# Performance work log

Measured on AMD Instinct MI355X. Metric: run time of the kernel, lower is better.

Reference implementation:

```python
import jax, jax.numpy as jnp
import numpy as np

C = 512
NH = 4
HD = C // NH
G = 32  # min(32, C) and C % 32 == 0
EPS = 1e-5


def setup_inputs() -> dict:
    key = jax.random.key(0)
    ks = jax.random.split(key, 11)
    s = 1.0 / np.sqrt(C)
    return {
        "x": jax.random.normal(ks[0], (16, C, 32, 32), dtype=jnp.float32),
        "gamma": jnp.ones((C,), jnp.float32),
        "beta": jnp.zeros((C,), jnp.float32),
        "wq": jax.random.normal(ks[1], (C, C), jnp.float32) * s,
        "bq": jax.random.normal(ks[2], (C,), jnp.float32) * 0.01,
        "wk": jax.random.normal(ks[3], (C, C), jnp.float32) * s,
        "bk": jax.random.normal(ks[4], (C,), jnp.float32) * 0.01,
        "wv": jax.random.normal(ks[5], (C, C), jnp.float32) * s,
        "bv": jax.random.normal(ks[6], (C,), jnp.float32) * 0.01,
        "wp": jax.random.normal(ks[7], (C, C), jnp.float32) * s,
        "bp": jax.random.normal(ks[8], (C,), jnp.float32) * 0.01,
    }


def _group_norm(x, gamma, beta):
    b, c, h, w = x.shape
    xr = x.reshape(b, G, c // G, h, w)
    mean = xr.mean(axis=(2, 3, 4), keepdims=True)
    var = xr.var(axis=(2, 3, 4), keepdims=True)
    xn = ((xr - mean) * jax.lax.rsqrt(var + EPS)).reshape(b, c, h, w)
    return xn * gamma[None, :, None, None] + beta[None, :, None, None]


def _conv1x1(x, w, b):
    # 1x1 conv == per-position channel GEMM
    return jnp.einsum('oc,bchw->bohw', w, x) + b[None, :, None, None]


def reference(x, gamma, beta, wq, bq, wk, bk, wv, bv, wp, bp):
    b, c, h, w = x.shape
    hw = h * w
    scale = HD ** (-0.5)
    hn = _group_norm(x, gamma, beta)
    q = _conv1x1(hn, wq, bq).reshape(b, NH, HD, hw)
    k = _conv1x1(hn, wk, bk).reshape(b, NH, HD, hw)
    v = _conv1x1(hn, wv, bv).reshape(b, NH, HD, hw)
    attn = jnp.einsum('bhdq,bhdk->bhqk', q, k) * scale  # [b, nh, hw, hw]
    attn = jax.nn.softmax(attn, axis=-1)
    out = jnp.einsum('bhqk,bhdk->bhdq', attn, v)  # [b, nh, hd, hw]
    out = out.reshape(b, c, h, w)
    out = _conv1x1(out, wp, bp)
    return x + out
```

## Files before the change

### kernel.cpp

```cpp
#include <hip/hip_runtime.h>
#include <math.h>

#define CCH 512
#define NH 4
#define HD 128
#define HW 1024
#define BATCH 16
#define EPS 1e-5f

typedef __attribute__((ext_vector_type(8))) short bfrag;
typedef __attribute__((ext_vector_type(4))) float f4;

static __device__ __forceinline__ unsigned short f2bf(float f) {
  union { float f; unsigned u; } v;
  v.f = f;
  unsigned r = v.u + 0x7fff + ((v.u >> 16) & 1);
  return (unsigned short)(r >> 16);
}
static __device__ __forceinline__ unsigned pack2(unsigned short a, unsigned short b) {
  return (unsigned)a | ((unsigned)b << 16);
}
static __device__ __forceinline__ void ldg_lds16(const unsigned short* g,
                                                 unsigned short* l) {
  __builtin_amdgcn_global_load_lds(
      (const __attribute__((address_space(1))) unsigned int*)g,
      (__attribute__((address_space(3))) unsigned int*)l, 16, 0, 0);
}

__global__ __launch_bounds__(256) void wcvt_kernel(const float* __restrict__ s0,
                                                   const float* __restrict__ s1,
                                                   const float* __restrict__ s2,
                                                   const float* __restrict__ s3,
                                                   unsigned short* __restrict__ d) {
  const float* srcs[4] = {s0, s1, s2, s3};
  const float* s = srcs[blockIdx.y];
  unsigned short* dp = d + (size_t)blockIdx.y * CCH * CCH;
  int i = blockIdx.x * 256 + threadIdx.x;
  f4 v = ((const f4*)s)[i];
  ushort4 o;
  o.x = f2bf(v.x); o.y = f2bf(v.y); o.z = f2bf(v.z); o.w = f2bf(v.w);
  ((ushort4*)dp)[i] = o;
}

__global__ __launch_bounds__(256) void gn_kernel(const float* __restrict__ x,
                                                 const float* __restrict__ gamma,
                                                 const float* __restrict__ beta,
                                                 unsigned short* __restrict__ hn) {
  int b = blockIdx.x >> 5, g = blockIdx.x & 31;
  const float* xp = x + ((size_t)b * CCH + g * 16) * HW;
  int t = threadIdx.x;
  float s = 0.f, ss = 0.f;
  const f4* xp4 = (const f4*)xp;
  for (int i = t; i < 4096; i += 256) {
    f4 v = xp4[i];
    s += v.x + v.y + v.z + v.w;
    ss += v.x * v.x + v.y * v.y + v.z * v.z + v.w * v.w;
  }
#pragma unroll
  for (int off = 32; off > 0; off >>= 1) {
    s += __shfl_xor(s, off);
    ss += __shfl_xor(ss, off);
  }
  __shared__ float rs[4], rss[4];
  int w = t >> 6;
  if ((t & 63) == 0) { rs[w] = s; rss[w] = ss; }
  __syncthreads();
  s = rs[0] + rs[1] + rs[2] + rs[3];
  ss = rss[0] + rss[1] + rss[2] + rss[3];
  const float invn = 1.f / (16 * HW);
  float mean = s * invn;
  float var = ss * invn - mean * mean;
  float rstd = rsqrtf(var + EPS);
  float a_[16], b_[16];
#pragma unroll
  for (int c = 0; c < 16; ++c) {
    float gm = gamma[g * 16 + c] * rstd;
    a_[c] = gm;
    b_[c] = beta[g * 16 + c] - mean * gm;
  }
#pragma unroll
  for (int i = 0; i < 4; ++i) {
    int p = t + 256 * i;
    unsigned short tv[16];
#pragma unroll
    for (int c = 0; c < 16; ++c) tv[c] = f2bf(xp[c * HW + p] * a_[c] + b_[c]);
    uint4 u0, u1;
    u0.x = pack2(tv[0], tv[1]);  u0.y = pack2(tv[2], tv[3]);
    u0.z = pack2(tv[4], tv[5]);  u0.w = pack2(tv[6], tv[7]);
    u1.x = pack2(tv[8], tv[9]);  u1.y = pack2(tv[10], tv[11]);
    u1.z = pack2(tv[12], tv[13]); u1.w = pack2(tv[14], tv[15]);
    unsigned short* dst = hn + ((size_t)b * HW + p) * CCH + g * 16;
    *(uint4*)dst = u0;
    *(uint4*)(dst + 8) = u1;
  }
}

template <int PROJ>
__global__ __launch_bounds__(256, 3) void mm_kernel(
    const unsigned short* __restrict__ Xt, const unsigned short* __restrict__ Wb,
    const float* __restrict__ b0, const float* __restrict__ b1,
    const float* __restrict__ b2, const float* __restrict__ resid,
    unsigned short* __restrict__ O0, unsigned short* __restrict__ O1,
    unsigned short* __restrict__ O2, float* __restrict__ Ofp) {
  int b = blockIdx.z;
  int p0 = blockIdx.x * 128;
  int c0g = blockIdx.y * 128;
  __shared__ __align__(16) unsigned short Xs[128 * 32];
  __shared__ __align__(16) unsigned short Ws[128 * 32];
  int t = threadIdx.x;
  int w = t >> 6, lane = t & 63, l15 = lane & 15, quad = lane >> 4;
  int wp = (w & 1) * 64, wc = (w >> 1) * 64;
  const unsigned short* Xb = Xt + (size_t)b * HW * CCH;
  const unsigned short* Wr = Wb + (size_t)c0g * CCH;
  f4 acc[4][4] = {};
  for (int k0 = 0; k0 < CCH; k0 += 32) {
    __syncthreads();
#pragma unroll
    for (int j = 0; j < 2; ++j) {
      int chk = w * 2 + j;
      int r = chk * 16 + (lane >> 2);
      int c = (lane & 3) ^ (r & 3);
      ldg_lds16(&Xb[(size_t)(p0 + r) * CCH + k0 + c * 8], &Xs[chk * 512]);
      ldg_lds16(&Wr[(size_t)r * CCH + k0 + c * 8], &Ws[chk * 512]);
    }
    __syncthreads();
    bfrag af[4], bf[4];
#pragma unroll
    for (int pt = 0; pt < 4; ++pt) {
      int r = wp + pt * 16 + l15;
      af[pt] = *(const bfrag*)&Xs[r * 32 + (quad ^ (r & 3)) * 8];
    }
#pragma unroll
    for (int ct = 0; ct < 4; ++ct) {
      int r = wc + ct * 16 + l15;
      bf[ct] = *(const bfrag*)&Ws[r * 32 + (quad ^ (r & 3)) * 8];
    }
#pragma unroll
    for (int pt = 0; pt < 4; ++pt)
#pragma unroll
      for (int ct = 0; ct < 4; ++ct)
        acc[pt][ct] = __builtin_amdgcn_mfma_f32_16x16x32_bf16(
            af[pt], bf[ct], acc[pt][ct], 0, 0, 0);
  }
  if (PROJ) {
#pragma unroll
    for (int ct = 0; ct < 4; ++ct) {
      int ch = c0g + wc + ct * 16 + l15;
      float bi = b0[ch];
#pragma unroll
      for (int pt = 0; pt < 4; ++pt) {
        int pos = p0 + wp + pt * 16 + quad * 4;
        f4 v = acc[pt][ct];
        size_t off = (size_t)b * CCH * HW + (size_t)ch * HW + pos;
        float4 rv = *(const float4*)&resid[off];
        float4 st;
        st.x = v.x + bi + rv.x; st.y = v.y + bi + rv.y;
        st.z = v.z + bi + rv.z; st.w = v.w + bi + rv.w;
        *(float4*)&Ofp[off] = st;
      }
    }
  } else {
    int mat = c0g >> 9;
    int c0 = c0g & 511;
    const float* bias = mat == 0 ? b0 : (mat == 1 ? b1 : b2);
    unsigned short* O = mat == 0 ? O0 : (mat == 1 ? O1 : O2);
#pragma unroll
    for (int ct = 0; ct < 4; ++ct) {
      int ch = c0 + wc + ct * 16 + l15;
      float bi = bias[ch];
#pragma unroll
      for (int pt = 0; pt < 4; ++pt) {
        int pos = p0 + wp + pt * 16 + quad * 4;
        f4 v = acc[pt][ct];
        if (mat < 2) {
          unsigned short* Op = O + (size_t)b * HW * CCH;
          Op[(size_t)(pos + 0) * CCH + ch] = f2bf(v.x + bi);
          Op[(size_t)(pos + 1) * CCH + ch] = f2bf(v.y + bi);
          Op[(size_t)(pos + 2) * CCH + ch] = f2bf(v.z + bi);
          Op[(size_t)(pos + 3) * CCH + ch] = f2bf(v.w + bi);
        } else {
          unsigned short* Op = O + (size_t)b * CCH * HW;
          ushort4 st;
          st.x = f2bf(v.x + bi); st.y = f2bf(v.y + bi);
          st.z = f2bf(v.z + bi); st.w = f2bf(v.w + bi);
          *(ushort4*)&Op[(size_t)ch * HW + pos] = st;
        }
      }
    }
  }
}

__global__ __launch_bounds__(512, 3) void attn_kernel(
    const unsigned short* __restrict__ Qt, const unsigned short* __restrict__ Kt,
    const unsigned short* __restrict__ Vc, unsigned short* __restrict__ Ot) {
  int bh = blockIdx.x;
  int b = bh >> 2, h = bh & 3;
  int q0 = blockIdx.y * 128;
  int t = threadIdx.x;
  int w = t >> 6, lane = t & 63, l15 = lane & 15, quad = lane >> 4;
  __shared__ __align__(16) unsigned short SA[64 * 128];
  __shared__ __align__(16) unsigned short Vs[128 * 64];
  int rq = w * 16 + l15;
  bfrag qf[4];
#pragma unroll
  for (int ks = 0; ks < 4; ++ks)
    qf[ks] = *(const bfrag*)&Qt[((size_t)b * HW + q0 + rq) * CCH +
                                h * HD + ks * 32 + quad * 8];
  f4 o[8] = {};
  float mrow = -1e30f, lrow = 0.f;
  const float scale = 0.08838834764831845f;
  for (int kt = 0; kt < 16; ++kt) {
    int kk0 = kt * 64;
    __syncthreads();
#pragma unroll
    for (int j = 0; j < 2; ++j) {
      int chk = w * 2 + j;
      int r = chk * 4 + (lane >> 4);
      int c = (lane & 15) ^ (r & 7);
      ldg_lds16(&Kt[((size_t)b * HW + kk0 + r) * CCH + h * HD + c * 8],
                &SA[chk * 512]);
    }
#pragma unroll
    for (int j = 0; j < 2; ++j) {
      int chk = w * 2 + j;
      int r = chk * 8 + (lane >> 3);
      int c = (lane & 7) ^ (r & 7);
      ldg_lds16(&Vc[((size_t)b * CCH + h * HD + r) * HW + kk0 + c * 8],
                &Vs[chk * 512]);
    }
    __syncthreads();
    f4 S[4] = {};
#pragma unroll
    for (int ks = 0; ks < 4; ++ks) {
      bfrag kf[4];
#pragma unroll
      for (int mt = 0; mt < 4; ++mt) {
        int r = mt * 16 + l15;
        int cc = (4 * ks + quad) ^ (r & 7);
        kf[mt] = *(const bfrag*)&SA[r * 128 + cc * 8];
      }
#pragma unroll
      for (int mt = 0; mt < 4; ++mt)
        S[mt] = __builtin_amdgcn_mfma_f32_16x16x32_bf16(kf[mt], qf[ks], S[mt],
                                                        0, 0, 0);
    }
    float vv[16];
#pragma unroll
    for (int mt = 0; mt < 4; ++mt)
#pragma unroll
      for (int r = 0; r < 4; ++r) vv[mt * 4 + r] = S[mt][r] * scale;
    float tm = vv[0];
#pragma unroll
    for (int i = 1; i < 16; ++i) tm = fmaxf(tm, vv[i]);
    tm = fmaxf(tm, __shfl_xor(tm, 16));
    tm = fmaxf(tm, __shfl_xor(tm, 32));
    float mnew = fmaxf(mrow, tm);
    float alpha = __expf(mrow - mnew);
    float sum = 0.f;
    unsigned short pk[16];
#pragma unroll
    for (int i = 0; i < 16; ++i) {
      float p = __expf(vv[i] - mnew);
      sum += p;
      pk[i] = f2bf(p);
    }
    sum += __shfl_xor(sum, 16);
    sum += __shfl_xor(sum, 32);
    lrow = lrow * alpha + sum;
    mrow = mnew;
#pragma unroll
    for (int dt = 0; dt < 8; ++dt) o[dt] *= alpha;
    unsigned pk2[8];
#pragma unroll
    for (int mt = 0; mt < 4; ++mt) {
      pk2[mt * 2 + 0] = pack2(pk[mt * 4 + 0], pk[mt * 4 + 1]);
      pk2[mt * 2 + 1] = pack2(pk[mt * 4 + 2], pk[mt * 4 + 3]);
    }
    __syncthreads();
#pragma unroll
    for (int mt = 0; mt < 4; ++mt) {
      int cc = (2 * mt + (quad >> 1)) ^ (rq & 7);
      uint2 u;
      u.x = pk2[mt * 2 + 0];
      u.y = pk2[mt * 2 + 1];
      *(uint2*)&SA[rq * 64 + cc * 8 + (quad & 1) * 4] = u;
    }
    __syncthreads();
#pragma unroll
    for (int ks = 0; ks < 2; ++ks) {
      int cq = (4 * ks + quad) ^ (rq & 7);
      bfrag pf = *(const bfrag*)&SA[rq * 64 + cq * 8];
#pragma unroll
      for (int dt = 0; dt < 8; ++dt) {
        int r = dt * 16 + l15;
        int cc = (4 * ks + quad) ^ (r & 7);
        bfrag vf = *(const bfrag*)&Vs[r * 64 + cc * 8];
        o[dt] = __builtin_amdgcn_mfma_f32_16x16x32_bf16(vf, pf, o[dt], 0, 0, 0);
      }
    }
  }
  float inv = 1.f / lrow;
  int q = q0 + rq;
#pragma unroll
  for (int dt = 0; dt < 8; ++dt) {
    f4 v = o[dt];
    ushort4 st;
    st.x = f2bf(v.x * inv); st.y = f2bf(v.y * inv);
    st.z = f2bf(v.z * inv); st.w = f2bf(v.w * inv);
    *(ushort4*)&Ot[((size_t)b * HW + q) * CCH + h * HD + dt * 16 + quad * 4] = st;
  }
}

extern "C" void kernel_launch(void* const* d_in, const int* in_sizes, int n_in,
                              void* d_out, int out_size, void* d_ws,
                              size_t ws_size, hipStream_t stream) {
  const float* x = (const float*)d_in[0];
  const float* gamma = (const float*)d_in[1];
  const float* beta = (const float*)d_in[2];
  const float* wq = (const float*)d_in[3];
  const float* bq = (const float*)d_in[4];
  const float* wk = (const float*)d_in[5];
  const float* bk = (const float*)d_in[6];
  const float* wv = (const float*)d_in[7];
  const float* bv = (const float*)d_in[8];
  const float* wp = (const float*)d_in[9];
  const float* bp = (const float*)d_in[10];

  const size_t TS = (size_t)BATCH * HW * CCH;
  unsigned short* wB = (unsigned short*)d_ws;
  unsigned short* hn = wB + (size_t)4 * CCH * CCH;
  unsigned short* Qt = hn + TS;
  unsigned short* Kt = Qt + TS;
  unsigned short* Vc = Kt + TS;
  unsigned short* Ot = hn;

  wcvt_kernel<<<dim3(256, 4), 256, 0, stream>>>(wq, wk, wv, wp, wB);
  gn_kernel<<<dim3(BATCH * 32), 256, 0, stream>>>(x, gamma, beta, hn);
  mm_kernel<0><<<dim3(8, 12, BATCH), 256, 0, stream>>>(
      hn, wB, bq, bk, bv, nullptr, Qt, Kt, Vc, nullptr);
  attn_kernel<<<dim3(64, 8), 512, 0, stream>>>(Qt, Kt, Vc, Ot);
  mm_kernel<1><<<dim3(8, 4, BATCH), 256, 0, stream>>>(
      Ot, wB + (size_t)3 * CCH * CCH, bp, bp, bp, x, nullptr, nullptr, nullptr,
      (float*)d_out);
}
```

Measured before the change: 240.2 us.

## Use 32x32 MFMA in attention with register P shuffle; vectorize Q/K stores

The attention kernel moves from 16x16x32 to 32x32x16 bf16 MFMA. Each wave now owns 32 query rows and the block drops to 256 threads. The probability matrix is rearranged between lane halves with cross-lane shuffles instead of a round trip through shared memory, which removes two barriers per key tile. The QKV GEMM swaps MFMA operands for the Q/K outputs so each lane holds four consecutive channels, turning four scalar bf16 stores into one 8-byte store. In exchange, per-thread register pressure rises and there are fewer waves per block.

Result: slower. 281.4 us (+17.2%).

```diff
diff --git a/kernel.cpp b/kernel.cpp
--- a/kernel.cpp
+++ b/kernel.cpp
@@ -10,6 +10,7 @@
 
 typedef __attribute__((ext_vector_type(8))) short bfrag;
 typedef __attribute__((ext_vector_type(4))) float f4;
+typedef __attribute__((ext_vector_type(16))) float f16v;
 
 static __device__ __forceinline__ unsigned short f2bf(float f) {
   union { float f; unsigned u; } v;
@@ -112,6 +113,7 @@
   int wp = (w & 1) * 64, wc = (w >> 1) * 64;
   const unsigned short* Xb = Xt + (size_t)b * HW * CCH;
   const unsigned short* Wr = Wb + (size_t)c0g * CCH;
+  const bool swap = (PROJ == 0) && (c0g < 1024);
   f4 acc[4][4] = {};
   for (int k0 = 0; k0 < CCH; k0 += 32) {
     __syncthreads();
@@ -135,12 +137,21 @@
       int r = wc + ct * 16 + l15;
       bf[ct] = *(const bfrag*)&Ws[r * 32 + (quad ^ (r & 3)) * 8];
     }
-#pragma unroll
-    for (int pt = 0; pt < 4; ++pt)
-#pragma unroll
-      for (int ct = 0; ct < 4; ++ct)
-        acc[pt][ct] = __builtin_amdgcn_mfma_f32_16x16x32_bf16(
-            af[pt], bf[ct], acc[pt][ct], 0, 0, 0);
+    if (swap) {
+#pragma unroll
+      for (int pt = 0; pt < 4; ++pt)
+#pragma unroll
+        for (int ct = 0; ct < 4; ++ct)
+          acc[pt][ct] = __builtin_amdgcn_mfma_f32_16x16x32_bf16(
+              bf[ct], af[pt], acc[pt][ct], 0, 0, 0);
+    } else {
+#pragma unroll
+      for (int pt = 0; pt < 4; ++pt)
+#pragma unroll
+        for (int ct = 0; ct < 4; ++ct)
+          acc[pt][ct] = __builtin_amdgcn_mfma_f32_16x16x32_bf16(
+              af[pt], bf[ct], acc[pt][ct], 0, 0, 0);
+    }
   }
   if (PROJ) {
 #pragma unroll
@@ -164,22 +175,32 @@
     int c0 = c0g & 511;
     const float* bias = mat == 0 ? b0 : (mat == 1 ? b1 : b2);
     unsigned short* O = mat == 0 ? O0 : (mat == 1 ? O1 : O2);
-#pragma unroll
-    for (int ct = 0; ct < 4; ++ct) {
-      int ch = c0 + wc + ct * 16 + l15;
-      float bi = bias[ch];
-#pragma unroll
-      for (int pt = 0; pt < 4; ++pt) {
-        int pos = p0 + wp + pt * 16 + quad * 4;
-        f4 v = acc[pt][ct];
-        if (mat < 2) {
-          unsigned short* Op = O + (size_t)b * HW * CCH;
-          Op[(size_t)(pos + 0) * CCH + ch] = f2bf(v.x + bi);
-          Op[(size_t)(pos + 1) * CCH + ch] = f2bf(v.y + bi);
-          Op[(size_t)(pos + 2) * CCH + ch] = f2bf(v.z + bi);
-          Op[(size_t)(pos + 3) * CCH + ch] = f2bf(v.w + bi);
-        } else {
-          unsigned short* Op = O + (size_t)b * CCH * HW;
+    if (mat < 2) {
+      unsigned short* Op = O + (size_t)b * HW * CCH;
+#pragma unroll
+      for (int ct = 0; ct < 4; ++ct) {
+        int ch0 = c0 + wc + ct * 16 + quad * 4;
+        float4 bi = *(const float4*)&bias[ch0];
+#pragma unroll
+        for (int pt = 0; pt < 4; ++pt) {
+          int pos = p0 + wp + pt * 16 + l15;
+          f4 v = acc[pt][ct];
+          ushort4 st;
+          st.x = f2bf(v.x + bi.x); st.y = f2bf(v.y + bi.y);
+          st.z = f2bf(v.z + bi.z); st.w = f2bf(v.w + bi.w);
+          *(ushort4*)&Op[(size_t)pos * CCH + ch0] = st;
+        }
+      }
+    } else {
+      unsigned short* Op = O + (size_t)b * CCH * HW;
+#pragma unroll
+      for (int ct = 0; ct < 4; ++ct) {
+        int ch = c0 + wc + ct * 16 + l15;
+        float bi = bias[ch];
+#pragma unroll
+        for (int pt = 0; pt < 4; ++pt) {
+          int pos = p0 + wp + pt * 16 + quad * 4;
+          f4 v = acc[pt][ct];
           ushort4 st;
           st.x = f2bf(v.x + bi); st.y = f2bf(v.y + bi);
           st.z = f2bf(v.z + bi); st.w = f2bf(v.w + bi);
@@ -190,125 +211,123 @@
   }
 }
 
-__global__ __launch_bounds__(512, 3) void attn_kernel(
+__global__ __launch_bounds__(256, 2) void attn_kernel(
     const unsigned short* __restrict__ Qt, const unsigned short* __restrict__ Kt,
     const unsigned short* __restrict__ Vc, unsigned short* __restrict__ Ot) {
   int bh = blockIdx.x;
   int b = bh >> 2, h = bh & 3;
   int q0 = blockIdx.y * 128;
   int t = threadIdx.x;
-  int w = t >> 6, lane = t & 63, l15 = lane & 15, quad = lane >> 4;
-  __shared__ __align__(16) unsigned short SA[64 * 128];
+  int w = t >> 6, lane = t & 63;
+  int l31 = lane & 31, half = lane >> 5;
+  __shared__ __align__(16) unsigned short Ks[64 * 128];
   __shared__ __align__(16) unsigned short Vs[128 * 64];
-  int rq = w * 16 + l15;
-  bfrag qf[4];
-#pragma unroll
-  for (int ks = 0; ks < 4; ++ks)
-    qf[ks] = *(const bfrag*)&Qt[((size_t)b * HW + q0 + rq) * CCH +
-                                h * HD + ks * 32 + quad * 8];
-  f4 o[8] = {};
+  int q = q0 + w * 32 + l31;
+  bfrag qf[8];
+#pragma unroll
+  for (int ks = 0; ks < 8; ++ks)
+    qf[ks] = *(const bfrag*)&Qt[((size_t)b * HW + q) * CCH + h * HD +
+                                ks * 16 + half * 8];
+  f16v o[4] = {};
   float mrow = -1e30f, lrow = 0.f;
   const float scale = 0.08838834764831845f;
   for (int kt = 0; kt < 16; ++kt) {
     int kk0 = kt * 64;
     __syncthreads();
 #pragma unroll
-    for (int j = 0; j < 2; ++j) {
-      int chk = w * 2 + j;
+    for (int j = 0; j < 4; ++j) {
+      int chk = w * 4 + j;
       int r = chk * 4 + (lane >> 4);
-      int c = (lane & 15) ^ (r & 7);
+      int c = (lane & 15) ^ (r & 15);
       ldg_lds16(&Kt[((size_t)b * HW + kk0 + r) * CCH + h * HD + c * 8],
-                &SA[chk * 512]);
-    }
-#pragma unroll
-    for (int j = 0; j < 2; ++j) {
-      int chk = w * 2 + j;
+                &Ks[chk * 512]);
+    }
+#pragma unroll
+    for (int j = 0; j < 4; ++j) {
+      int chk = w * 4 + j;
       int r = chk * 8 + (lane >> 3);
       int c = (lane & 7) ^ (r & 7);
       ldg_lds16(&Vc[((size_t)b * CCH + h * HD + r) * HW + kk0 + c * 8],
                 &Vs[chk * 512]);
     }
     __syncthreads();
-    f4 S[4] = {};
-#pragma unroll
-    for (int ks = 0; ks < 4; ++ks) {
-      bfrag kf[4];
-#pragma unroll
-      for (int mt = 0; mt < 4; ++mt) {
-        int r = mt * 16 + l15;
-        int cc = (4 * ks + quad) ^ (r & 7);
-        kf[mt] = *(const bfrag*)&SA[r * 128 + cc * 8];
-      }
-#pragma unroll
-      for (int mt = 0; mt < 4; ++mt)
-        S[mt] = __builtin_amdgcn_mfma_f32_16x16x32_bf16(kf[mt], qf[ks], S[mt],
+    f16v S[2] = {};
+#pragma unroll
+    for (int ks = 0; ks < 8; ++ks) {
+      int c16 = ks * 2 + half;
+#pragma unroll
+      for (int mt = 0; mt < 2; ++mt) {
+        int r = mt * 32 + l31;
+        bfrag kf = *(const bfrag*)&Ks[r * 128 + ((c16 ^ (r & 15)) << 3)];
+        S[mt] = __builtin_amdgcn_mfma_f32_32x32x16_bf16(kf, qf[ks], S[mt],
                                                         0, 0, 0);
-    }
-    float vv[16];
-#pragma unroll
-    for (int mt = 0; mt < 4; ++mt)
-#pragma unroll
-      for (int r = 0; r < 4; ++r) vv[mt * 4 + r] = S[mt][r] * scale;
+      }
+    }
+    float vv[32];
+#pragma unroll
+    for (int mt = 0; mt < 2; ++mt)
+#pragma unroll
+      for (int i = 0; i < 16; ++i) vv[mt * 16 + i] = S[mt][i] * scale;
     float tm = vv[0];
 #pragma unroll
-    for (int i = 1; i < 16; ++i) tm = fmaxf(tm, vv[i]);
-    tm = fmaxf(tm, __shfl_xor(tm, 16));
+    for (int i = 1; i < 32; ++i) tm = fmaxf(tm, vv[i]);
     tm = fmaxf(tm, __shfl_xor(tm, 32));
     float mnew = fmaxf(mrow, tm);
     float alpha = __expf(mrow - mnew);
     float sum = 0.f;
-    unsigned short pk[16];
+    unsigned pd[16];
 #pragma unroll
     for (int i = 0; i < 16; ++i) {
-      float p = __expf(vv[i] - mnew);
-      sum += p;
-      pk[i] = f2bf(p);
-    }
-    sum += __shfl_xor(sum, 16);
+      float p0 = __expf(vv[2 * i] - mnew);
+      float p1 = __expf(vv[2 * i + 1] - mnew);
+      sum += p0 + p1;
+      pd[i] = pack2(f2bf(p0), f2bf(p1));
+    }
     sum += __shfl_xor(sum, 32);
     lrow = lrow * alpha + sum;
     mrow = mnew;
 #pragma unroll
-    for (int dt = 0; dt < 8; ++dt) o[dt] *= alpha;
-    unsigned pk2[8];
-#pragma unroll
-    for (int mt = 0; mt < 4; ++mt) {
-      pk2[mt * 2 + 0] = pack2(pk[mt * 4 + 0], pk[mt * 4 + 1]);
-      pk2[mt * 2 + 1] = pack2(pk[mt * 4 + 2], pk[mt * 4 + 3]);
-    }
-    __syncthreads();
-#pragma unroll
-    for (int mt = 0; mt < 4; ++mt) {
-      int cc = (2 * mt + (quad >> 1)) ^ (rq & 7);
-      uint2 u;
-      u.x = pk2[mt * 2 + 0];
-      u.y = pk2[mt * 2 + 1];
-      *(uint2*)&SA[rq * 64 + cc * 8 + (quad & 1) * 4] = u;
-    }
-    __syncthreads();
-#pragma unroll
-    for (int ks = 0; ks < 2; ++ks) {
-      int cq = (4 * ks + quad) ^ (rq & 7);
-      bfrag pf = *(const bfrag*)&SA[rq * 64 + cq * 8];
-#pragma unroll
-      for (int dt = 0; dt < 8; ++dt) {
-        int r = dt * 16 + l15;
-        int cc = (4 * ks + quad) ^ (r & 7);
-        bfrag vf = *(const bfrag*)&Vs[r * 64 + cc * 8];
-        o[dt] = __builtin_amdgcn_mfma_f32_16x16x32_bf16(vf, pf, o[dt], 0, 0, 0);
-      }
-    }
+    for (int dt = 0; dt < 4; ++dt)
+#pragma unroll
+      for (int i = 0; i < 16; ++i) o[dt][i] *= alpha;
+#pragma unroll
+    for (int mt = 0; mt < 2; ++mt)
+#pragma unroll
+      for (int s = 0; s < 2; ++s) {
+        int base = mt * 8 + s * 4;
+        unsigned s0 = half ? pd[base + 0] : pd[base + 2];
+        unsigned s1 = half ? pd[base + 1] : pd[base + 3];
+        unsigned r0 = (unsigned)__shfl_xor((int)s0, 32);
+        unsigned r1 = (unsigned)__shfl_xor((int)s1, 32);
+        union { unsigned u[4]; bfrag f; } pf;
+        pf.u[0] = half ? r0 : pd[base + 0];
+        pf.u[1] = half ? r1 : pd[base + 1];
+        pf.u[2] = half ? pd[base + 2] : r0;
+        pf.u[3] = half ? pd[base + 3] : r1;
+        int c8 = (mt * 2 + s) * 2 + half;
+#pragma unroll
+        for (int dt = 0; dt < 4; ++dt) {
+          int r = dt * 32 + l31;
+          bfrag vf = *(const bfrag*)&Vs[r * 64 + ((c8 ^ (r & 7)) << 3)];
+          o[dt] = __builtin_amdgcn_mfma_f32_32x32x16_bf16(vf, pf.f, o[dt],
+                                                          0, 0, 0);
+        }
+      }
   }
   float inv = 1.f / lrow;
-  int q = q0 + rq;
-#pragma unroll
-  for (int dt = 0; dt < 8; ++dt) {
-    f4 v = o[dt];
-    ushort4 st;
-    st.x = f2bf(v.x * inv); st.y = f2bf(v.y * inv);
-    st.z = f2bf(v.z * inv); st.w = f2bf(v.w * inv);
-    *(ushort4*)&Ot[((size_t)b * HW + q) * CCH + h * HD + dt * 16 + quad * 4] = st;
-  }
+  unsigned short* Op = Ot + ((size_t)b * HW + q) * CCH + h * HD;
+#pragma unroll
+  for (int dt = 0; dt < 4; ++dt)
+#pragma unroll
+    for (int rg = 0; rg < 4; ++rg) {
+      int d = dt * 32 + rg * 8 + half * 4;
+      ushort4 st;
+      st.x = f2bf(o[dt][rg * 4 + 0] * inv);
+      st.y = f2bf(o[dt][rg * 4 + 1] * inv);
+      st.z = f2bf(o[dt][rg * 4 + 2] * inv);
+      st.w = f2bf(o[dt][rg * 4 + 3] * inv);
+      *(ushort4*)&Op[d] = st;
+    }
 }
 
 extern "C" void kernel_launch(void* const* d_in, const int* in_sizes, int n_in,
@@ -338,7 +357,7 @@
   gn_kernel<<<dim3(BATCH * 32), 256, 0, stream>>>(x, gamma, beta, hn);
   mm_kernel<0><<<dim3(8, 12, BATCH), 256, 0, stream>>>(
       hn, wB, bq, bk, bv, nullptr, Qt, Kt, Vc, nullptr);
-  attn_kernel<<<dim3(64, 8), 512, 0, stream>>>(Qt, Kt, Vc, Ot);
+  attn_kernel<<<dim3(64, 8), 256, 0, stream>>>(Qt, Kt, Vc, Ot);
   mm_kernel<1><<<dim3(8, 4, BATCH), 256, 0, stream>>>(
       Ot, wB + (size_t)3 * CCH * CCH, bp, bp, bp, x, nullptr, nullptr, nullptr,
       (float*)d_out);
```
